# Optimization experiments

Measured on AMD Instinct MI355X. Metric: run time of the kernel, lower is better.

The kernel has to match this reference:

```python
import jax, jax.numpy as jnp
import numpy as np

N_NODES = 150000   # n_users + n_entities
N_EDGES = 4800000  # nnz of sparse A_in (avg degree 32)
EMBED_DIM = 64
CONV_DIMS = [64, 32, 16]  # [embed_dim] + conv_dim_list
EPS = 1e-12  # F.normalize eps


def setup_inputs() -> dict:
    key = jax.random.key(0)
    ks = jax.random.split(key, 12)
    inp = {
        "E": jax.random.normal(ks[0], (N_NODES, EMBED_DIM), jnp.float32) * 0.1,
        "edge_vals": jax.random.uniform(ks[1], (N_EDGES,), jnp.float32),
        "rows": jax.random.randint(ks[2], (N_EDGES,), 0, N_NODES),
        "cols": jax.random.randint(ks[3], (N_EDGES,), 0, N_NODES),
    }
    i = 4
    for l in range(len(CONV_DIMS) - 1):
        din, dout = CONV_DIMS[l], CONV_DIMS[l + 1]
        scale = 1.0 / np.sqrt(din)
        inp[f"W1_{l}"] = jax.random.normal(ks[i], (dout, din), jnp.float32) * scale
        inp[f"b1_{l}"] = jax.random.normal(ks[i + 1], (dout,), jnp.float32) * 0.01
        inp[f"W2_{l}"] = jax.random.normal(ks[i + 2], (dout, din), jnp.float32) * scale
        inp[f"b2_{l}"] = jax.random.normal(ks[i + 3], (dout,), jnp.float32) * 0.01
        i += 4
    return inp


def _cf_embeddings(E, edge_vals, rows, cols, layer_params):
    """UIR_KG.calc_cf_embeddings: sparse A_in @ x, then KGAT bi-interaction."""
    N = E.shape[0]
    x = E
    outs = [x]
    for (W1, b1, W2, b2) in layer_params:
        # side = A_in @ x  as gather -> weight -> scatter-add over COO edges
        msgs = edge_vals[:, None] * x[cols]              # [n_edges, d]
        side = jax.ops.segment_sum(msgs, rows, num_segments=N)  # [N, d]
        sum_emb = jax.nn.leaky_relu((x + side) @ W1.T + b1)     # Linear1 + LeakyReLU
        bi_emb = jax.nn.leaky_relu((x * side) @ W2.T + b2)      # Linear2 + LeakyReLU
        x = sum_emb + bi_emb
        norm = jnp.linalg.norm(x, axis=1, keepdims=True)        # F.normalize(p=2, dim=1)
        outs.append(x / jnp.maximum(norm, EPS))
    return jnp.concatenate(outs, axis=1)  # [N, 64+32+16]


def reference(E, edge_vals, W1_0, b1_0, W2_0, b2_0, W1_1, b1_1, W2_1, b2_1, rows, cols):
    params = [(W1_0, b1_0, W2_0, b2_0), (W1_1, b1_1, W2_1, b2_1)]
    return _cf_embeddings(E, edge_vals, rows, cols, params)
```

## Files before the change

### kernel.cpp

```cpp
#include <hip/hip_runtime.h>


constexpr int PSHIFT = 9;
constexpr int PROWS  = 1 << PSHIFT;
constexpr int PBINS  = 512;
constexpr int GF_T   = 1024;
constexpr int GF_E   = 4096;
constexpr int GF_K   = GF_E / GF_T;

static __device__ __forceinline__ float leaky(float v) {
    return v > 0.0f ? v : 0.01f * v;
}

static __device__ __forceinline__ unsigned short f2bf_rne(float f) {
    unsigned u = __float_as_uint(f);
    return (unsigned short)((u + 0x7FFF + ((u >> 16) & 1)) >> 16);
}

static __device__ __forceinline__ void unpack2(unsigned u, float& lo, float& hi) {
    lo = __uint_as_float(u << 16);
    hi = __uint_as_float(u & 0xFFFF0000u);
}

static __device__ __forceinline__ unsigned pack2(float lo, float hi) {
    return ((unsigned)f2bf_rne(hi) << 16) | (unsigned)f2bf_rne(lo);
}

__global__ void copy_E_kernel(const float* __restrict__ E, float* __restrict__ out,
                              unsigned short* __restrict__ Ebf, int N) {
    int tid = blockIdx.x * blockDim.x + threadIdx.x;
    if (tid >= N * 16) return;
    int i = tid >> 4, g = tid & 15;
    float4 v = reinterpret_cast<const float4*>(E)[(size_t)i * 16 + g];
    *reinterpret_cast<float4*>(out + (size_t)i * 112 + g * 4) = v;
    if (Ebf) {
        ushort4 b;
        b.x = f2bf_rne(v.x); b.y = f2bf_rne(v.y);
        b.z = f2bf_rne(v.z); b.w = f2bf_rne(v.w);
        *reinterpret_cast<ushort4*>(Ebf + (size_t)i * 64 + g * 4) = b;
    }
}

__global__ void part_hist_kernel(const int* __restrict__ rows, int* __restrict__ pcnt,
                                 int NE, int P) {
    extern __shared__ int h[];
    for (int i = threadIdx.x; i < P; i += blockDim.x) h[i] = 0;
    __syncthreads();
    for (int e = blockIdx.x * blockDim.x + threadIdx.x; e < NE; e += gridDim.x * blockDim.x)
        atomicAdd(&h[rows[e] >> PSHIFT], 1);
    __syncthreads();
    for (int i = threadIdx.x; i < P; i += blockDim.x) {
        int c = h[i];
        if (c) atomicAdd(&pcnt[i], c);
    }
}

__global__ __launch_bounds__(PBINS) void part_scan_kernel(
    const int* __restrict__ pcnt, int* __restrict__ pbase,
    int* __restrict__ gcur, int P, int NE) {
    __shared__ int s[PBINS];
    int v = (threadIdx.x < (unsigned)P) ? pcnt[threadIdx.x] : 0;
    s[threadIdx.x] = v;
    __syncthreads();
    for (int off = 1; off < PBINS; off <<= 1) {
        int t = (threadIdx.x >= (unsigned)off) ? s[threadIdx.x - off] : 0;
        __syncthreads();
        s[threadIdx.x] += t;
        __syncthreads();
    }
    if (threadIdx.x < (unsigned)P) {
        int ex = s[threadIdx.x] - v;
        pbase[threadIdx.x] = ex;
        gcur[threadIdx.x]  = ex;
    }
    if (threadIdx.x == 0) pbase[P] = NE;
}

__global__ __launch_bounds__(GF_T) void group_flush_kernel(
    const int* __restrict__ rows, const int* __restrict__ cols,
    const float* __restrict__ ev, int* __restrict__ gcur,
    int2* __restrict__ tmp, int NE, int P) {
    __shared__ int2 staged[GF_E];
    __shared__ unsigned short sp[GF_E];
    __shared__ int hist[PBINS], runstart[PBINS], hcur[PBINS], gbase[PBINS], scanb[PBINS];

    int e0  = blockIdx.x * GF_E;
    int cnt = min(GF_E, NE - e0);

    if (threadIdx.x < PBINS) hist[threadIdx.x] = 0;
    __syncthreads();

    int pk[GF_K], ck[GF_K], rk[GF_K];
    float vk[GF_K];
#pragma unroll
    for (int k = 0; k < GF_K; k++) {
        int idx = threadIdx.x + k * GF_T;
        if (idx < cnt) {
            int r = rows[e0 + idx];
            pk[k] = r >> PSHIFT;
            rk[k] = r & (PROWS - 1);
            ck[k] = cols[e0 + idx];
            vk[k] = ev[e0 + idx];
            atomicAdd(&hist[pk[k]], 1);
        } else pk[k] = -1;
    }
    __syncthreads();
    if (threadIdx.x < PBINS) scanb[threadIdx.x] = hist[threadIdx.x];
    __syncthreads();
    for (int off = 1; off < PBINS; off <<= 1) {
        int t = 0;
        if (threadIdx.x < PBINS && threadIdx.x >= (unsigned)off) t = scanb[threadIdx.x - off];
        __syncthreads();
        if (threadIdx.x < PBINS) scanb[threadIdx.x] += t;
        __syncthreads();
    }
    if (threadIdx.x < PBINS) {
        int ex = scanb[threadIdx.x] - hist[threadIdx.x];
        runstart[threadIdx.x] = ex;
        hcur[threadIdx.x]     = ex;
    }
    __syncthreads();
#pragma unroll
    for (int k = 0; k < GF_K; k++) {
        if (pk[k] >= 0) {
            int slot = atomicAdd(&hcur[pk[k]], 1);
            staged[slot] = make_int2(ck[k] | (rk[k] << 18), __float_as_int(vk[k]));
            sp[slot] = (unsigned short)pk[k];
        }
    }
    __syncthreads();
    if (threadIdx.x < (unsigned)P) {
        int h = hist[threadIdx.x];
        if (h > 0) gbase[threadIdx.x] = atomicAdd(&gcur[threadIdx.x], h);
    }
    __syncthreads();
#pragma unroll
    for (int k = 0; k < GF_K; k++) {
        int i = threadIdx.x + k * GF_T;
        if (i < cnt) {
            int p = sp[i];
            tmp[gbase[p] + (i - runstart[p])] = staged[i];
        }
    }
}

__global__ __launch_bounds__(PROWS) void row_sort_kernel(
    const int2* __restrict__ tmp, int2* __restrict__ pairs,
    const int* __restrict__ pbase, int* __restrict__ row_end, int N) {
    __shared__ int hist[PROWS], cur[PROWS], scanb[PROWS];
    int p     = blockIdx.x;
    int start = pbase[p];
    int end   = pbase[p + 1];
    hist[threadIdx.x] = 0;
    __syncthreads();
    for (int e = start + threadIdx.x; e < end; e += PROWS)
        atomicAdd(&hist[tmp[e].x >> 18], 1);
    __syncthreads();
    scanb[threadIdx.x] = hist[threadIdx.x];
    __syncthreads();
    for (int off = 1; off < PROWS; off <<= 1) {
        int t = (threadIdx.x >= (unsigned)off) ? scanb[threadIdx.x - off] : 0;
        __syncthreads();
        scanb[threadIdx.x] += t;
        __syncthreads();
    }
    int inc = scanb[threadIdx.x];
    cur[threadIdx.x] = start + inc - hist[threadIdx.x];
    int row = (p << PSHIFT) + threadIdx.x;
    if (row < N) row_end[row] = start + inc;
    __syncthreads();
    for (int e = start + threadIdx.x; e < end; e += PROWS) {
        int2 t = tmp[e];
        int pos = atomicAdd(&cur[t.x >> 18], 1);
        pairs[pos] = make_int2(t.x & 0x3FFFF, t.y);
    }
}

template<int DIN, int DOUT>
__global__ __launch_bounds__(256) void pull_layer_b2_kernel(
    const unsigned short* __restrict__ xb,
    const int2* __restrict__ pairs, const int* __restrict__ row_end,
    const float* __restrict__ W1, const float* __restrict__ b1,
    const float* __restrict__ W2, const float* __restrict__ b2,
    unsigned short* __restrict__ xnextb,
    float* __restrict__ out, int out_col0, int N) {
    constexpr int Q   = DIN / 8;
    constexpr int RPB = 256 / Q;
    constexpr int JT  = DOUT / Q;
    constexpr int LDU = DIN + 8;
    constexpr int LDW = DIN + 4;
    static_assert(JT == 4, "thread owns 4 outputs");

    __shared__ float sW1[DOUT * LDW];
    __shared__ float sW2[DOUT * LDW];
    __shared__ unsigned short hb[2][RPB][LDU];

    for (int idx = threadIdx.x; idx < DOUT * DIN; idx += 256) {
        int j = idx / DIN, k = idx % DIN;
        sW1[j * LDW + k] = W1[idx];
        sW2[j * LDW + k] = W2[idx];
    }

    int lr  = threadIdx.x / Q;
    int q   = threadIdx.x % Q;
    int row = blockIdx.x * RPB + lr;

    if (row < N) {
        int start = row ? row_end[row - 1] : 0;
        int end   = row_end[row];
        const uint4* xbv = reinterpret_cast<const uint4*>(xb);
        float acc[8] = {0.f, 0.f, 0.f, 0.f, 0.f, 0.f, 0.f, 0.f};
        int e = start;
        for (; e + 3 < end; e += 4) {
            int2 p[4]; uint4 g[4];
#pragma unroll
            for (int k = 0; k < 4; k++) p[k] = pairs[e + k];
#pragma unroll
            for (int k = 0; k < 4; k++) g[k] = xbv[(size_t)p[k].x * Q + q];
#pragma unroll
            for (int k = 0; k < 4; k++) {
                float v = __int_as_float(p[k].y);
                float lo, hi;
                unpack2(g[k].x, lo, hi); acc[0] += v * lo; acc[1] += v * hi;
                unpack2(g[k].y, lo, hi); acc[2] += v * lo; acc[3] += v * hi;
                unpack2(g[k].z, lo, hi); acc[4] += v * lo; acc[5] += v * hi;
                unpack2(g[k].w, lo, hi); acc[6] += v * lo; acc[7] += v * hi;
            }
        }
        for (; e < end; e++) {
            int2 p0 = pairs[e];
            uint4 g0 = xbv[(size_t)p0.x * Q + q];
            float v0 = __int_as_float(p0.y);
            float lo, hi;
            unpack2(g0.x, lo, hi); acc[0] += v0 * lo; acc[1] += v0 * hi;
            unpack2(g0.y, lo, hi); acc[2] += v0 * lo; acc[3] += v0 * hi;
            unpack2(g0.z, lo, hi); acc[4] += v0 * lo; acc[5] += v0 * hi;
            unpack2(g0.w, lo, hi); acc[6] += v0 * lo; acc[7] += v0 * hi;
        }
        uint4 xr = xbv[(size_t)row * Q + q];
        float xf[8];
        unpack2(xr.x, xf[0], xf[1]);
        unpack2(xr.y, xf[2], xf[3]);
        unpack2(xr.z, xf[4], xf[5]);
        unpack2(xr.w, xf[6], xf[7]);
        uint4 s1, s2;
        s1.x = pack2(xf[0] + acc[0], xf[1] + acc[1]);
        s1.y = pack2(xf[2] + acc[2], xf[3] + acc[3]);
        s1.z = pack2(xf[4] + acc[4], xf[5] + acc[5]);
        s1.w = pack2(xf[6] + acc[6], xf[7] + acc[7]);
        s2.x = pack2(xf[0] * acc[0], xf[1] * acc[1]);
        s2.y = pack2(xf[2] * acc[2], xf[3] * acc[3]);
        s2.z = pack2(xf[4] * acc[4], xf[5] * acc[5]);
        s2.w = pack2(xf[6] * acc[6], xf[7] * acc[7]);
        *reinterpret_cast<uint4*>(&hb[0][lr][q * 8]) = s1;
        *reinterpret_cast<uint4*>(&hb[1][lr][q * 8]) = s2;
    }
    __syncthreads();
    if (row >= N) return;

    float a1[4], a2[4];
#pragma unroll
    for (int jj = 0; jj < 4; jj++) {
        a1[jj] = b1[q + Q * jj];
        a2[jj] = b2[q + Q * jj];
    }
    const uint4* h1r = reinterpret_cast<const uint4*>(&hb[0][lr][0]);
    const uint4* h2r = reinterpret_cast<const uint4*>(&hb[1][lr][0]);
#pragma unroll
    for (int c = 0; c < DIN / 8; c++) {
        uint4 u1 = h1r[c], u2 = h2r[c];
        float f1[8], f2[8];
        unpack2(u1.x, f1[0], f1[1]); unpack2(u1.y, f1[2], f1[3]);
        unpack2(u1.z, f1[4], f1[5]); unpack2(u1.w, f1[6], f1[7]);
        unpack2(u2.x, f2[0], f2[1]); unpack2(u2.y, f2[2], f2[3]);
        unpack2(u2.z, f2[4], f2[5]); unpack2(u2.w, f2[6], f2[7]);
#pragma unroll
        for (int jj = 0; jj < 4; jj++) {
            int j = q + Q * jj;
            const float4* w1p = reinterpret_cast<const float4*>(&sW1[j * LDW + c * 8]);
            const float4* w2p = reinterpret_cast<const float4*>(&sW2[j * LDW + c * 8]);
            float4 wa = w1p[0], wb = w1p[1];
            float4 wc = w2p[0], wd = w2p[1];
            a1[jj] += f1[0] * wa.x + f1[1] * wa.y + f1[2] * wa.z + f1[3] * wa.w
                    + f1[4] * wb.x + f1[5] * wb.y + f1[6] * wb.z + f1[7] * wb.w;
            a2[jj] += f2[0] * wc.x + f2[1] * wc.y + f2[2] * wc.z + f2[3] * wc.w
                    + f2[4] * wd.x + f2[5] * wd.y + f2[6] * wd.z + f2[7] * wd.w;
        }
    }
    float y[4], nrm = 0.f;
#pragma unroll
    for (int jj = 0; jj < 4; jj++) {
        y[jj] = leaky(a1[jj]) + leaky(a2[jj]);
        nrm += y[jj] * y[jj];
    }
#pragma unroll
    for (int m = 1; m < Q; m <<= 1) nrm += __shfl_xor(nrm, m, 64);
    float inv = 1.0f / fmaxf(sqrtf(nrm), 1e-12f);
    if (xnextb) {
#pragma unroll
        for (int jj = 0; jj < 4; jj++)
            xnextb[(size_t)row * DOUT + q + Q * jj] = f2bf_rne(y[jj]);
    }
    float* o = out + (size_t)row * 112 + out_col0;
#pragma unroll
    for (int jj = 0; jj < 4; jj++) o[q + Q * jj] = y[jj] * inv;
}

template<int DIN, int DOUT>
__global__ __launch_bounds__(256) void pull_layer_kernel(
    const float* __restrict__ x, const int2* __restrict__ pairs,
    const int* __restrict__ row_end,
    const float* __restrict__ W1, const float* __restrict__ b1,
    const float* __restrict__ W2, const float* __restrict__ b2,
    float* __restrict__ xnext, float* __restrict__ out, int out_col0, int N) {
    constexpr int Q   = DIN / 4;
    constexpr int RPB = 256 / Q;
    constexpr int LD  = DIN + 4;
    constexpr int LD4 = LD / 4;
    static_assert(DOUT == 2 * Q, "thread owns exactly 2 output dims");

    __shared__ float sW1[DOUT * LD];
    __shared__ float sW2[DOUT * LD];
    __shared__ float hb[2][RPB][LD];

    for (int idx = threadIdx.x; idx < DOUT * DIN; idx += 256) {
        int j = idx / DIN, k = idx % DIN;
        sW1[j * LD + k] = W1[idx];
        sW2[j * LD + k] = W2[idx];
    }

    int lr  = threadIdx.x / Q;
    int q   = threadIdx.x % Q;
    int row = blockIdx.x * RPB + lr;

    if (row < N) {
        int start = row ? row_end[row - 1] : 0;
        int end   = row_end[row];
        const float4* xv = reinterpret_cast<const float4*>(x);
        float4 acc = make_float4(0.f, 0.f, 0.f, 0.f);
        int e = start;
        for (; e + 3 < end; e += 4) {
            int2 p0 = pairs[e];
            int2 p1 = pairs[e + 1];
            int2 p2 = pairs[e + 2];
            int2 p3 = pairs[e + 3];
            float4 g0 = xv[(size_t)p0.x * Q + q];
            float4 g1 = xv[(size_t)p1.x * Q + q];
            float4 g2 = xv[(size_t)p2.x * Q + q];
            float4 g3 = xv[(size_t)p3.x * Q + q];
            float v0 = __int_as_float(p0.y), v1 = __int_as_float(p1.y);
            float v2 = __int_as_float(p2.y), v3 = __int_as_float(p3.y);
            acc.x += v0 * g0.x; acc.y += v0 * g0.y; acc.z += v0 * g0.z; acc.w += v0 * g0.w;
            acc.x += v1 * g1.x; acc.y += v1 * g1.y; acc.z += v1 * g1.z; acc.w += v1 * g1.w;
            acc.x += v2 * g2.x; acc.y += v2 * g2.y; acc.z += v2 * g2.z; acc.w += v2 * g2.w;
            acc.x += v3 * g3.x; acc.y += v3 * g3.y; acc.z += v3 * g3.z; acc.w += v3 * g3.w;
        }
        for (; e < end; e++) {
            int2 p0 = pairs[e];
            float4 g0 = xv[(size_t)p0.x * Q + q];
            float v0 = __int_as_float(p0.y);
            acc.x += v0 * g0.x; acc.y += v0 * g0.y; acc.z += v0 * g0.z; acc.w += v0 * g0.w;
        }
        float4 xr = xv[(size_t)row * Q + q];
        float4 h1 = make_float4(xr.x + acc.x, xr.y + acc.y, xr.z + acc.z, xr.w + acc.w);
        float4 h2 = make_float4(xr.x * acc.x, xr.y * acc.y, xr.z * acc.z, xr.w * acc.w);
        *reinterpret_cast<float4*>(&hb[0][lr][q * 4]) = h1;
        *reinterpret_cast<float4*>(&hb[1][lr][q * 4]) = h2;
    }
    __syncthreads();
    if (row >= N) return;

    float a0 = b1[q], a1 = b1[q + Q], a2 = b2[q], a3 = b2[q + Q];
    const float4* w1v = reinterpret_cast<const float4*>(sW1);
    const float4* w2v = reinterpret_cast<const float4*>(sW2);
    const float4* h1v = reinterpret_cast<const float4*>(&hb[0][lr][0]);
    const float4* h2v = reinterpret_cast<const float4*>(&hb[1][lr][0]);
#pragma unroll
    for (int k4 = 0; k4 < DIN / 4; k4++) {
        float4 h1 = h1v[k4];
        float4 h2 = h2v[k4];
        float4 wa = w1v[q * LD4 + k4];
        float4 wb = w1v[(q + Q) * LD4 + k4];
        float4 wc = w2v[q * LD4 + k4];
        float4 wd = w2v[(q + Q) * LD4 + k4];
        a0 += h1.x * wa.x + h1.y * wa.y + h1.z * wa.z + h1.w * wa.w;
        a1 += h1.x * wb.x + h1.y * wb.y + h1.z * wb.z + h1.w * wb.w;
        a2 += h2.x * wc.x + h2.y * wc.y + h2.z * wc.z + h2.w * wc.w;
        a3 += h2.x * wd.x + h2.y * wd.y + h2.z * wd.z + h2.w * wd.w;
    }
    float y0 = leaky(a0) + leaky(a2);
    float y1 = leaky(a1) + leaky(a3);
    float nrm = y0 * y0 + y1 * y1;
#pragma unroll
    for (int m = 1; m < Q; m <<= 1) nrm += __shfl_xor(nrm, m, 64);
    float inv = 1.0f / fmaxf(sqrtf(nrm), 1e-12f);
    if (xnext) {
        xnext[(size_t)row * DOUT + q]     = y0;
        xnext[(size_t)row * DOUT + q + Q] = y1;
    }
    float* o = out + (size_t)row * 112 + out_col0;
    o[q]     = y0 * inv;
    o[q + Q] = y1 * inv;
}

extern "C" void kernel_launch(void* const* d_in, const int* in_sizes, int n_in,
                              void* d_out, int out_size, void* d_ws, size_t ws_size,
                              hipStream_t stream) {
    const float* Eemb = (const float*)d_in[0];
    const float* ev   = (const float*)d_in[1];
    const int*   rows = (const int*)d_in[2];
    const int*   cols = (const int*)d_in[3];
    const float* W1_0 = (const float*)d_in[4];
    const float* b1_0 = (const float*)d_in[5];
    const float* W2_0 = (const float*)d_in[6];
    const float* b2_0 = (const float*)d_in[7];
    const float* W1_1 = (const float*)d_in[8];
    const float* b1_1 = (const float*)d_in[9];
    const float* W2_1 = (const float*)d_in[10];
    const float* b2_1 = (const float*)d_in[11];
    float* out = (float*)d_out;

    int N  = in_sizes[0] / 64;
    int NE = in_sizes[1];
    int P  = (N + PROWS - 1) >> PSHIFT;

    size_t pairs_b  = (size_t)NE * sizeof(int2);
    size_t rowend_b = ((size_t)N * sizeof(int) + 255) & ~(size_t)255;
    size_t small_b  = (PBINS + (PBINS + 1) + PBINS) * sizeof(int) + 256;
    small_b = (small_b + 255) & ~(size_t)255;
    size_t ebf_b    = ((size_t)N * 64 * sizeof(unsigned short) + 255) & ~(size_t)255;
    size_t x1b_b    = (size_t)N * 32 * sizeof(unsigned short);

    char* base = (char*)d_ws;
    int2*  pairs   = (int2*)base;
    int*   row_end = (int*)(base + pairs_b);
    int*   pcnt    = (int*)(base + pairs_b + rowend_b);
    int*   pbase   = pcnt + PBINS;
    int*   gcur    = pbase + PBINS + 1;
    unsigned short* Ebf = (unsigned short*)(base + pairs_b + rowend_b + small_b);
    unsigned short* x1b = (unsigned short*)(base + pairs_b + rowend_b + small_b + ebf_b);
    float* x1 = (float*)(base + pairs_b + rowend_b + small_b);

    bool use_bf = ws_size >= pairs_b + rowend_b + small_b + ebf_b + x1b_b;

    int2* tmp = (int2*)d_out;

    hipMemsetAsync(pcnt, 0, PBINS * sizeof(int), stream);
    part_hist_kernel<<<256, 1024, P * sizeof(int), stream>>>(rows, pcnt, NE, P);
    part_scan_kernel<<<1, PBINS, 0, stream>>>(pcnt, pbase, gcur, P, NE);
    group_flush_kernel<<<(NE + GF_E - 1) / GF_E, GF_T, 0, stream>>>(
        rows, cols, ev, gcur, tmp, NE, P);
    row_sort_kernel<<<P, PROWS, 0, stream>>>(tmp, pairs, pbase, row_end, N);

    copy_E_kernel<<<(N * 16 + 255) / 256, 256, 0, stream>>>(
        Eemb, out, use_bf ? Ebf : nullptr, N);

    if (use_bf) {
        pull_layer_b2_kernel<64, 32><<<(N + 31) / 32, 256, 0, stream>>>(
            Ebf, pairs, row_end, W1_0, b1_0, W2_0, b2_0, x1b, out, 64, N);
        pull_layer_b2_kernel<32, 16><<<(N + 63) / 64, 256, 0, stream>>>(
            x1b, pairs, row_end, W1_1, b1_1, W2_1, b2_1, nullptr, out, 96, N);
    } else {
        pull_layer_kernel<64, 32><<<(N + 15) / 16, 256, 0, stream>>>(
            Eemb, pairs, row_end, W1_0, b1_0, W2_0, b2_0, x1, out, 64, N);
        pull_layer_kernel<32, 16><<<(N + 31) / 32, 256, 0, stream>>>(
            x1, pairs, row_end, W1_1, b1_1, W2_1, b2_1, nullptr, out, 96, N);
    }
}
```

Baseline: 341.5 us.

## Sort rows by degree to balance work in pull-layer kernels

Adds a degree histogram, scan and scatter pass that builds a permutation of rows grouped by in-degree, and the two bf16 pull-layer kernels now process rows in that order. The aim is to cut wavefront divergence and tail imbalance, since rows sharing a block then have similar edge counts. In exchange it adds three small kernels and a memset, uses global atomics in the scatter, and the permuted row order scatters output writes and x-row accesses, which loses locality.

After: 638.5 us. 1.87x slower.

```diff
diff --git a/kernel.cpp b/kernel.cpp
--- a/kernel.cpp
+++ b/kernel.cpp
@@ -176,20 +176,56 @@
     }
 }
 
+__global__ void deg_hist_kernel(const int* __restrict__ row_end,
+                                int* __restrict__ dcnt, int N) {
+    __shared__ int h[256];
+    h[threadIdx.x] = 0;
+    __syncthreads();
+    for (int r = blockIdx.x * blockDim.x + threadIdx.x; r < N; r += gridDim.x * blockDim.x) {
+        int d = row_end[r] - (r ? row_end[r - 1] : 0);
+        atomicAdd(&h[min(d, 255)], 1);
+    }
+    __syncthreads();
+    int c = h[threadIdx.x];
+    if (c) atomicAdd(&dcnt[threadIdx.x], c);
+}
+
+__global__ void deg_scan_kernel(const int* __restrict__ dcnt, int* __restrict__ dcur) {
+    __shared__ int s[256];
+    int v = dcnt[threadIdx.x];
+    s[threadIdx.x] = v;
+    __syncthreads();
+    for (int off = 1; off < 256; off <<= 1) {
+        int t = (threadIdx.x >= (unsigned)off) ? s[threadIdx.x - off] : 0;
+        __syncthreads();
+        s[threadIdx.x] += t;
+        __syncthreads();
+    }
+    dcur[threadIdx.x] = s[threadIdx.x] - v;
+}
+
+__global__ void deg_scatter_kernel(const int* __restrict__ row_end, int* __restrict__ dcur,
+                                   int* __restrict__ perm, int N) {
+    int r = blockIdx.x * blockDim.x + threadIdx.x;
+    if (r >= N) return;
+    int d = row_end[r] - (r ? row_end[r - 1] : 0);
+    int pos = atomicAdd(&dcur[min(d, 255)], 1);
+    perm[pos] = r;
+}
+
 template<int DIN, int DOUT>
 __global__ __launch_bounds__(256) void pull_layer_b2_kernel(
     const unsigned short* __restrict__ xb,
     const int2* __restrict__ pairs, const int* __restrict__ row_end,
+    const int* __restrict__ perm,
     const float* __restrict__ W1, const float* __restrict__ b1,
     const float* __restrict__ W2, const float* __restrict__ b2,
     unsigned short* __restrict__ xnextb,
     float* __restrict__ out, int out_col0, int N) {
     constexpr int Q   = DIN / 8;
     constexpr int RPB = 256 / Q;
-    constexpr int JT  = DOUT / Q;
     constexpr int LDU = DIN + 8;
     constexpr int LDW = DIN + 4;
-    static_assert(JT == 4, "thread owns 4 outputs");
 
     __shared__ float sW1[DOUT * LDW];
     __shared__ float sW2[DOUT * LDW];
@@ -203,9 +239,10 @@
 
     int lr  = threadIdx.x / Q;
     int q   = threadIdx.x % Q;
-    int row = blockIdx.x * RPB + lr;
-
-    if (row < N) {
+    int idx = blockIdx.x * RPB + lr;
+    int row = (idx < N) ? perm[idx] : -1;
+
+    if (row >= 0) {
         int start = row ? row_end[row - 1] : 0;
         int end   = row_end[row];
         const uint4* xbv = reinterpret_cast<const uint4*>(xb);
@@ -256,7 +293,7 @@
         *reinterpret_cast<uint4*>(&hb[1][lr][q * 8]) = s2;
     }
     __syncthreads();
-    if (row >= N) return;
+    if (row < 0) return;
 
     float a1[4], a2[4];
 #pragma unroll
@@ -426,10 +463,11 @@
 
     size_t pairs_b  = (size_t)NE * sizeof(int2);
     size_t rowend_b = ((size_t)N * sizeof(int) + 255) & ~(size_t)255;
-    size_t small_b  = (PBINS + (PBINS + 1) + PBINS) * sizeof(int) + 256;
+    size_t small_b  = (PBINS + (PBINS + 1) + PBINS + 256 + 256) * sizeof(int) + 256;
     small_b = (small_b + 255) & ~(size_t)255;
     size_t ebf_b    = ((size_t)N * 64 * sizeof(unsigned short) + 255) & ~(size_t)255;
-    size_t x1b_b    = (size_t)N * 32 * sizeof(unsigned short);
+    size_t x1b_b    = ((size_t)N * 32 * sizeof(unsigned short) + 255) & ~(size_t)255;
+    size_t perm_b   = (size_t)N * sizeof(int);
 
     char* base = (char*)d_ws;
     int2*  pairs   = (int2*)base;
@@ -437,15 +475,19 @@
     int*   pcnt    = (int*)(base + pairs_b + rowend_b);
     int*   pbase   = pcnt + PBINS;
     int*   gcur    = pbase + PBINS + 1;
+    int*   dcnt    = gcur + PBINS;
+    int*   dcur    = dcnt + 256;
     unsigned short* Ebf = (unsigned short*)(base + pairs_b + rowend_b + small_b);
     unsigned short* x1b = (unsigned short*)(base + pairs_b + rowend_b + small_b + ebf_b);
-    float* x1 = (float*)(base + pairs_b + rowend_b + small_b);
-
-    bool use_bf = ws_size >= pairs_b + rowend_b + small_b + ebf_b + x1b_b;
+    int*   perm    = (int*)(base + pairs_b + rowend_b + small_b + ebf_b + x1b_b);
+    float* x1      = (float*)(base + pairs_b + rowend_b + small_b);
+
+    bool use_bf = ws_size >= pairs_b + rowend_b + small_b + ebf_b + x1b_b + perm_b;
 
     int2* tmp = (int2*)d_out;
 
     hipMemsetAsync(pcnt, 0, PBINS * sizeof(int), stream);
+    hipMemsetAsync(dcnt, 0, 256 * sizeof(int), stream);
     part_hist_kernel<<<256, 1024, P * sizeof(int), stream>>>(rows, pcnt, NE, P);
     part_scan_kernel<<<1, PBINS, 0, stream>>>(pcnt, pbase, gcur, P, NE);
     group_flush_kernel<<<(NE + GF_E - 1) / GF_E, GF_T, 0, stream>>>(
@@ -456,10 +498,14 @@
         Eemb, out, use_bf ? Ebf : nullptr, N);
 
     if (use_bf) {
+        deg_hist_kernel<<<256, 256, 0, stream>>>(row_end, dcnt, N);
+        deg_scan_kernel<<<1, 256, 0, stream>>>(dcnt, dcur);
+        deg_scatter_kernel<<<(N + 255) / 256, 256, 0, stream>>>(row_end, dcur, perm, N);
+
         pull_layer_b2_kernel<64, 32><<<(N + 31) / 32, 256, 0, stream>>>(
-            Ebf, pairs, row_end, W1_0, b1_0, W2_0, b2_0, x1b, out, 64, N);
+            Ebf, pairs, row_end, perm, W1_0, b1_0, W2_0, b2_0, x1b, out, 64, N);
         pull_layer_b2_kernel<32, 16><<<(N + 63) / 64, 256, 0, stream>>>(
-            x1b, pairs, row_end, W1_1, b1_1, W2_1, b2_1, nullptr, out, 96, N);
+            x1b, pairs, row_end, perm, W1_1, b1_1, W2_1, b2_1, nullptr, out, 96, N);
     } else {
         pull_layer_kernel<64, 32><<<(N + 15) / 16, 256, 0, stream>>>(
             Eemb, pairs, row_end, W1_0, b1_0, W2_0, b2_0, x1, out, 64, N);
```

## Reorder rows by degree within partitions to balance pull-layer wavefronts

Applied to the files above, without the earlier changes.

The row sort kernel now also builds a per-partition permutation of rows, using a shared-memory counting sort over in-degree capped at 255. Both bf16 pull layers process rows through this permutation, so rows of similar degree share a wavefront. The aim is to reduce lane divergence and idle time from variable-length edge loops. The cost is an extra indirection, scattered output and row-state writes in permuted order, a bit more work in the sort kernel, and a fallback path that passes row_end as the perm buffer.

After: 358.8 us. +5.1%, slower.

```diff
diff --git a/kernel.cpp b/kernel.cpp
--- a/kernel.cpp
+++ b/kernel.cpp
@@ -146,30 +146,55 @@
 
 __global__ __launch_bounds__(PROWS) void row_sort_kernel(
     const int2* __restrict__ tmp, int2* __restrict__ pairs,
-    const int* __restrict__ pbase, int* __restrict__ row_end, int N) {
+    const int* __restrict__ pbase, int* __restrict__ row_end,
+    int* __restrict__ perm, int N) {
     __shared__ int hist[PROWS], cur[PROWS], scanb[PROWS];
+    __shared__ int dh[256], dbase[256];
     int p     = blockIdx.x;
     int start = pbase[p];
     int end   = pbase[p + 1];
-    hist[threadIdx.x] = 0;
-    __syncthreads();
-    for (int e = start + threadIdx.x; e < end; e += PROWS)
+    int tid   = threadIdx.x;
+    hist[tid] = 0;
+    if (tid < 256) dh[tid] = 0;
+    __syncthreads();
+    for (int e = start + tid; e < end; e += PROWS)
         atomicAdd(&hist[tmp[e].x >> 18], 1);
     __syncthreads();
-    scanb[threadIdx.x] = hist[threadIdx.x];
+    scanb[tid] = hist[tid];
     __syncthreads();
     for (int off = 1; off < PROWS; off <<= 1) {
-        int t = (threadIdx.x >= (unsigned)off) ? scanb[threadIdx.x - off] : 0;
-        __syncthreads();
-        scanb[threadIdx.x] += t;
-        __syncthreads();
-    }
-    int inc = scanb[threadIdx.x];
-    cur[threadIdx.x] = start + inc - hist[threadIdx.x];
-    int row = (p << PSHIFT) + threadIdx.x;
-    if (row < N) row_end[row] = start + inc;
-    __syncthreads();
-    for (int e = start + threadIdx.x; e < end; e += PROWS) {
+        int t = (tid >= (unsigned)off) ? scanb[tid - off] : 0;
+        __syncthreads();
+        scanb[tid] += t;
+        __syncthreads();
+    }
+    int inc = scanb[tid];
+    cur[tid] = start + inc - hist[tid];
+    int row = (p << PSHIFT) + tid;
+    bool valid = row < N;
+    if (valid) row_end[row] = start + inc;
+
+    int bin = min(hist[tid], 255);
+    if (valid) atomicAdd(&dh[bin], 1);
+    __syncthreads();
+    if (tid < 256) scanb[tid] = dh[tid];
+    __syncthreads();
+    for (int off = 1; off < 256; off <<= 1) {
+        int t = 0;
+        if (tid < 256 && tid >= (unsigned)off) t = scanb[tid - off];
+        __syncthreads();
+        if (tid < 256) scanb[tid] += t;
+        __syncthreads();
+    }
+    if (tid < 256) dbase[tid] = scanb[tid] - dh[tid];
+    __syncthreads();
+    if (valid) {
+        int slot = atomicAdd(&dbase[bin], 1);
+        perm[(p << PSHIFT) + slot] = row;
+    }
+    __syncthreads();
+
+    for (int e = start + tid; e < end; e += PROWS) {
         int2 t = tmp[e];
         int pos = atomicAdd(&cur[t.x >> 18], 1);
         pairs[pos] = make_int2(t.x & 0x3FFFF, t.y);
@@ -180,16 +205,15 @@
 __global__ __launch_bounds__(256) void pull_layer_b2_kernel(
     const unsigned short* __restrict__ xb,
     const int2* __restrict__ pairs, const int* __restrict__ row_end,
+    const int* __restrict__ perm,
     const float* __restrict__ W1, const float* __restrict__ b1,
     const float* __restrict__ W2, const float* __restrict__ b2,
     unsigned short* __restrict__ xnextb,
     float* __restrict__ out, int out_col0, int N) {
     constexpr int Q   = DIN / 8;
     constexpr int RPB = 256 / Q;
-    constexpr int JT  = DOUT / Q;
     constexpr int LDU = DIN + 8;
     constexpr int LDW = DIN + 4;
-    static_assert(JT == 4, "thread owns 4 outputs");
 
     __shared__ float sW1[DOUT * LDW];
     __shared__ float sW2[DOUT * LDW];
@@ -203,9 +227,10 @@
 
     int lr  = threadIdx.x / Q;
     int q   = threadIdx.x % Q;
-    int row = blockIdx.x * RPB + lr;
-
-    if (row < N) {
+    int idx = blockIdx.x * RPB + lr;
+    int row = (idx < N) ? perm[idx] : -1;
+
+    if (row >= 0) {
         int start = row ? row_end[row - 1] : 0;
         int end   = row_end[row];
         const uint4* xbv = reinterpret_cast<const uint4*>(xb);
@@ -256,7 +281,7 @@
         *reinterpret_cast<uint4*>(&hb[1][lr][q * 8]) = s2;
     }
     __syncthreads();
-    if (row >= N) return;
+    if (row < 0) return;
 
     float a1[4], a2[4];
 #pragma unroll
@@ -429,7 +454,8 @@
     size_t small_b  = (PBINS + (PBINS + 1) + PBINS) * sizeof(int) + 256;
     small_b = (small_b + 255) & ~(size_t)255;
     size_t ebf_b    = ((size_t)N * 64 * sizeof(unsigned short) + 255) & ~(size_t)255;
-    size_t x1b_b    = (size_t)N * 32 * sizeof(unsigned short);
+    size_t x1b_b    = ((size_t)N * 32 * sizeof(unsigned short) + 255) & ~(size_t)255;
+    size_t perm_b   = (size_t)N * sizeof(int);
 
     char* base = (char*)d_ws;
     int2*  pairs   = (int2*)base;
@@ -439,9 +465,10 @@
     int*   gcur    = pbase + PBINS + 1;
     unsigned short* Ebf = (unsigned short*)(base + pairs_b + rowend_b + small_b);
     unsigned short* x1b = (unsigned short*)(base + pairs_b + rowend_b + small_b + ebf_b);
-    float* x1 = (float*)(base + pairs_b + rowend_b + small_b);
-
-    bool use_bf = ws_size >= pairs_b + rowend_b + small_b + ebf_b + x1b_b;
+    int*   perm    = (int*)(base + pairs_b + rowend_b + small_b + ebf_b + x1b_b);
+    float* x1      = (float*)(base + pairs_b + rowend_b + small_b);
+
+    bool use_bf = ws_size >= pairs_b + rowend_b + small_b + ebf_b + x1b_b + perm_b;
 
     int2* tmp = (int2*)d_out;
 
@@ -450,16 +477,17 @@
     part_scan_kernel<<<1, PBINS, 0, stream>>>(pcnt, pbase, gcur, P, NE);
     group_flush_kernel<<<(NE + GF_E - 1) / GF_E, GF_T, 0, stream>>>(
         rows, cols, ev, gcur, tmp, NE, P);
-    row_sort_kernel<<<P, PROWS, 0, stream>>>(tmp, pairs, pbase, row_end, N);
+    row_sort_kernel<<<P, PROWS, 0, stream>>>(tmp, pairs, pbase, row_end,
+                                             use_bf ? perm : row_end , N);
 
     copy_E_kernel<<<(N * 16 + 255) / 256, 256, 0, stream>>>(
         Eemb, out, use_bf ? Ebf : nullptr, N);
 
     if (use_bf) {
         pull_layer_b2_kernel<64, 32><<<(N + 31) / 32, 256, 0, stream>>>(
-            Ebf, pairs, row_end, W1_0, b1_0, W2_0, b2_0, x1b, out, 64, N);
+            Ebf, pairs, row_end, perm, W1_0, b1_0, W2_0, b2_0, x1b, out, 64, N);
         pull_layer_b2_kernel<32, 16><<<(N + 63) / 64, 256, 0, stream>>>(
-            x1b, pairs, row_end, W1_1, b1_1, W2_1, b2_1, nullptr, out, 96, N);
+            x1b, pairs, row_end, perm, W1_1, b1_1, W2_1, b2_1, nullptr, out, 96, N);
     } else {
         pull_layer_kernel<64, 32><<<(N + 15) / 16, 256, 0, stream>>>(
             Eemb, pairs, row_end, W1_0, b1_0, W2_0, b2_0, x1, out, 64, N);
```
